# Optimization experiments

Measured on AMD Instinct MI355X. Metric: run time of the kernel, lower is better.

The kernel has to match this reference:

```python
import jax, jax.numpy as jnp
import numpy as np

LOSS_WEIGHT = 1.0


def _pairwise_l1(x, y):
    # x: [B, N, 3], y: [B, M, 3] -> d: [B, N, M] with d[b,i,j] = sum_k |x[b,i,k]-y[b,j,k]|
    # Loop over the fixed D=3 coordinate axis to avoid a [B,N,M,3] intermediate.
    d = jnp.abs(x[:, :, None, 0] - y[:, None, :, 0])
    for k in range(1, x.shape[-1]):
        d = d + jnp.abs(x[:, :, None, k] - y[:, None, :, k])
    return d


def setup_inputs() -> dict:
    key = jax.random.key(0)
    kx, ky = jax.random.split(key)
    mesh_x = jax.random.normal(kx, (4, 4096, 3), dtype=jnp.float32)
    mesh_y = jax.random.normal(ky, (4, 4096, 3), dtype=jnp.float32)
    return {"mesh_x": mesh_x, "mesh_y": mesh_y}


def reference(mesh_x, mesh_y):
    # pytorch3d chamfer_distance(norm=1), point_reduction='mean', batch_reduction='mean'
    d = _pairwise_l1(mesh_x, mesh_y)          # [B, N, M]
    cham_x = jnp.min(d, axis=2)               # [B, N] nearest y for each x
    cham_y = jnp.min(d, axis=1)               # [B, M] nearest x for each y
    # mean over points then mean over batch == global mean (uniform N, M)
    loss = jnp.mean(cham_x) + jnp.mean(cham_y)
    return LOSS_WEIGHT * loss
```

## Files before the change

kernel.cpp:

```cpp
#include <hip/hip_runtime.h>

#define BATCH 4
#define NPTS  4096
#define TPB   64
#define PPT   4
#define PB    (TPB * PPT)
#define QC    128
#define ZMAX  32

__device__ __forceinline__ void min3(float& m, float a, float b) {
    asm("v_min3_f32 %0, %0, %1, %2" : "+v"(m) : "v"(a), "v"(b));
}

__global__ __launch_bounds__(TPB) void chamfer_all(const float* __restrict__ X,
                                                   const float* __restrict__ Y,
                                                   float* __restrict__ pmin,
                                                   float* __restrict__ out,
                                                   int zsteps) {
    if (blockIdx.x == 0 && blockIdx.y == 0 && blockIdx.z == 0 && threadIdx.x == 0)
        out[0] = 0.0f;

    const int dir = blockIdx.y >> 2;
    const int b   = blockIdx.y & 3;
    const int z   = blockIdx.z;
    const float* __restrict__ P = dir ? Y : X;
    const float* __restrict__ Q = dir ? X : Y;

    float px[PPT], py[PPT], pz[PPT], m[PPT];
    const int i0 = blockIdx.x * PB + threadIdx.x;
    #pragma unroll
    for (int u = 0; u < PPT; ++u) {
        const float* Pp = P + ((size_t)b * NPTS + i0 + u * TPB) * 3;
        px[u] = Pp[0];
        py[u] = Pp[1];
        pz[u] = Pp[2];
        m[u]  = __builtin_inff();
    }

    __shared__ float4 sq[QC];
    const int q0 = z * zsteps * QC;

    for (int s = 0; s < zsteps; ++s) {
        __syncthreads();
        const float* __restrict__ Qb = Q + ((size_t)b * NPTS + q0 + s * QC) * 3;
        for (int k = threadIdx.x; k < QC; k += TPB)
            sq[k] = make_float4(Qb[3 * k], Qb[3 * k + 1], Qb[3 * k + 2], 0.0f);
        __syncthreads();

        #pragma unroll 4
        for (int j = 0; j < QC; j += 2) {
            const float4 qa = sq[j];
            const float4 qb = sq[j + 1];
            #pragma unroll
            for (int u = 0; u < PPT; ++u) {
                float d0 = fabsf(px[u] - qa.x) + fabsf(py[u] - qa.y) + fabsf(pz[u] - qa.z);
                float d1 = fabsf(px[u] - qb.x) + fabsf(py[u] - qb.y) + fabsf(pz[u] - qb.z);
                min3(m[u], d0, d1);
            }
        }
    }

    float* dst = pmin + ((size_t)dir * gridDim.z + z) * (BATCH * NPTS) + b * NPTS + i0;
    #pragma unroll
    for (int u = 0; u < PPT; ++u) dst[u * TPB] = m[u];
}

__global__ __launch_bounds__(256) void reduce_loss(const float* __restrict__ pmin,
                                                   float* __restrict__ out, int Z) {
    const int half = BATCH * NPTS;
    const int s    = blockIdx.x * 256 + threadIdx.x;
    const int dir  = s >> 14;
    const int idx  = s & (half - 1);

    const float* __restrict__ base = pmin + (size_t)dir * Z * half + idx;
    float v = base[0];
    for (int z = 1; z < Z; ++z) v = fminf(v, base[(size_t)z * half]);

    for (int off = 32; off > 0; off >>= 1) v += __shfl_down(v, off, 64);

    __shared__ float partial[4];
    if ((threadIdx.x & 63) == 0) partial[threadIdx.x >> 6] = v;
    __syncthreads();
    if (threadIdx.x == 0) {
        float t = (partial[0] + partial[1] + partial[2] + partial[3]) *
                  (1.0f / (float)half);
        atomicAdd(out, t);
    }
}

extern "C" void kernel_launch(void* const* d_in, const int* in_sizes, int n_in,
                              void* d_out, int out_size, void* d_ws, size_t ws_size,
                              hipStream_t stream) {
    const float* X = (const float*)d_in[0];
    const float* Y = (const float*)d_in[1];
    float* out = (float*)d_out;
    float* pmin = (float*)d_ws;

    int Z = ZMAX;
    while (Z > 1 && (size_t)2 * Z * BATCH * NPTS * sizeof(float) > ws_size) Z >>= 1;
    const int zsteps = ZMAX / Z;

    dim3 grid(NPTS / PB, 2 * BATCH, Z);
    chamfer_all<<<grid, TPB, 0, stream>>>(X, Y, pmin, out, zsteps);

    reduce_loss<<<(2 * BATCH * NPTS) / 256, 256, 0, stream>>>(pmin, out, Z);
}
```

Before: 78.32 us.

## Fuse chamfer min and loss reduction into one kernel with last-block finalize

Replaces the two-kernel design (per-slice partial mins written to workspace, then a reduce kernel) with one kernel. Each 512-thread block covers 64 points against all query slices, split across 32 groups of 16 threads. The groups combine through shared-memory atomicMin, and a last-block-done counter performs the final sum. Query points are read directly from global memory as packed float4 instead of being staged in LDS. The distance uses v_add_f32 with abs modifiers. This removes the pmin workspace traffic and the second launch, at the cost of a memset launch, uncoalesced/redundant global Q reads, and an atomic counter.

```diff
diff --git a/kernel.cpp b/kernel.cpp
--- a/kernel.cpp
+++ b/kernel.cpp
@@ -2,89 +2,112 @@
 
 #define BATCH 4
 #define NPTS  4096
-#define TPB   64
+#define TPB   512
+#define PC    64
+#define NPG   16
 #define PPT   4
-#define PB    (TPB * PPT)
-#define QC    128
-#define ZMAX  32
+#define NZZ   32
+#define QSL   (NPTS / NZZ)
+#define NBLK  (2 * BATCH * (NPTS / PC))
 
 __device__ __forceinline__ void min3(float& m, float a, float b) {
     asm("v_min3_f32 %0, %0, %1, %2" : "+v"(m) : "v"(a), "v"(b));
 }
+__device__ __forceinline__ float add_abs2(float a, float b) {
+    float d;
+    asm("v_add_f32 %0, |%1|, |%2|" : "=v"(d) : "v"(a), "v"(b));
+    return d;
+}
+__device__ __forceinline__ float add_abs1(float acc, float c) {
+    float d;
+    asm("v_add_f32 %0, %1, |%2|" : "=v"(d) : "v"(acc), "v"(c));
+    return d;
+}
 
-__global__ __launch_bounds__(TPB) void chamfer_all(const float* __restrict__ X,
-                                                   const float* __restrict__ Y,
-                                                   float* __restrict__ pmin,
-                                                   float* __restrict__ out,
-                                                   int zsteps) {
-    if (blockIdx.x == 0 && blockIdx.y == 0 && blockIdx.z == 0 && threadIdx.x == 0)
-        out[0] = 0.0f;
-
-    const int dir = blockIdx.y >> 2;
-    const int b   = blockIdx.y & 3;
-    const int z   = blockIdx.z;
-    const float* __restrict__ P = dir ? Y : X;
-    const float* __restrict__ Q = dir ? X : Y;
-
-    float px[PPT], py[PPT], pz[PPT], m[PPT];
-    const int i0 = blockIdx.x * PB + threadIdx.x;
+__device__ __forceinline__ void dist4x4(const float4 g0, const float4 g1,
+                                        const float4 g2, const float px[PPT],
+                                        const float py[PPT], const float pz[PPT],
+                                        float m[PPT]) {
     #pragma unroll
     for (int u = 0; u < PPT; ++u) {
-        const float* Pp = P + ((size_t)b * NPTS + i0 + u * TPB) * 3;
-        px[u] = Pp[0];
-        py[u] = Pp[1];
-        pz[u] = Pp[2];
-        m[u]  = __builtin_inff();
+        float dA = add_abs1(add_abs2(px[u] - g0.x, py[u] - g0.y), pz[u] - g0.z);
+        float dB = add_abs1(add_abs2(px[u] - g0.w, py[u] - g1.x), pz[u] - g1.y);
+        float dC = add_abs1(add_abs2(px[u] - g1.z, py[u] - g1.w), pz[u] - g2.x);
+        float dD = add_abs1(add_abs2(px[u] - g2.y, py[u] - g2.z), pz[u] - g2.w);
+        min3(m[u], dA, dB);
+        min3(m[u], dC, dD);
+    }
+}
+
+__global__ __launch_bounds__(TPB) void chamfer_fused(const float* __restrict__ X,
+                                                     const float* __restrict__ Y,
+                                                     unsigned int* __restrict__ cnt,
+                                                     float* __restrict__ psum,
+                                                     float* __restrict__ out) {
+    const int t   = threadIdx.x;
+    const int pg  = t & (NPG - 1);
+    const int zz  = t >> 4;
+    const int bid = blockIdx.x;
+    const int x   = bid & 63;
+    const int db  = bid >> 6;
+    const int b   = db & 3;
+    const float* __restrict__ P = (db >> 2) ? Y : X;
+    const float* __restrict__ Q = (db >> 2) ? X : Y;
+
+    const float4* __restrict__ Ps =
+        (const float4*)(P + ((size_t)b * NPTS + x * PC + pg * PPT) * 3);
+    const float4 f0 = Ps[0], f1 = Ps[1], f2 = Ps[2];
+    float px[PPT], py[PPT], pz[PPT], m[PPT];
+    px[0]=f0.x; py[0]=f0.y; pz[0]=f0.z;  px[1]=f0.w; py[1]=f1.x; pz[1]=f1.y;
+    px[2]=f1.z; py[2]=f1.w; pz[2]=f2.x;  px[3]=f2.y; py[3]=f2.z; pz[3]=f2.w;
+    #pragma unroll
+    for (int u = 0; u < PPT; ++u) m[u] = __builtin_inff();
+
+    const float4* __restrict__ Qs =
+        (const float4*)(Q + ((size_t)b * NPTS + zz * QSL) * 3);
+    #pragma unroll 4
+    for (int j = 0; j < (QSL / 4) * 3; j += 3) {
+        const float4 g0 = Qs[j], g1 = Qs[j + 1], g2 = Qs[j + 2];
+        dist4x4(g0, g1, g2, px, py, pz, m);
     }
 
-    __shared__ float4 sq[QC];
-    const int q0 = z * zsteps * QC;
+    __shared__ unsigned int smin[PC];
+    __shared__ int lastf;
+    if (t < PC) smin[t] = 0x7F800000u;
+    __syncthreads();
+    #pragma unroll
+    for (int u = 0; u < PPT; ++u)
+        atomicMin(&smin[pg * PPT + u], __float_as_uint(m[u]));
+    __syncthreads();
 
-    for (int s = 0; s < zsteps; ++s) {
-        __syncthreads();
-        const float* __restrict__ Qb = Q + ((size_t)b * NPTS + q0 + s * QC) * 3;
-        for (int k = threadIdx.x; k < QC; k += TPB)
-            sq[k] = make_float4(Qb[3 * k], Qb[3 * k + 1], Qb[3 * k + 2], 0.0f);
-        __syncthreads();
-
-        #pragma unroll 4
-        for (int j = 0; j < QC; j += 2) {
-            const float4 qa = sq[j];
-            const float4 qb = sq[j + 1];
-            #pragma unroll
-            for (int u = 0; u < PPT; ++u) {
-                float d0 = fabsf(px[u] - qa.x) + fabsf(py[u] - qa.y) + fabsf(pz[u] - qa.z);
-                float d1 = fabsf(px[u] - qb.x) + fabsf(py[u] - qb.y) + fabsf(pz[u] - qb.z);
-                min3(m[u], d0, d1);
-            }
+    if (t < 64) {
+        float v = __uint_as_float(smin[t]);
+        #pragma unroll
+        for (int off = 32; off > 0; off >>= 1) v += __shfl_down(v, off, 64);
+        if (t == 0) {
+            __hip_atomic_store(&psum[bid], v, __ATOMIC_RELEASE,
+                               __HIP_MEMORY_SCOPE_AGENT);
+            unsigned int old = __hip_atomic_fetch_add(
+                cnt, 1u, __ATOMIC_ACQ_REL, __HIP_MEMORY_SCOPE_AGENT);
+            lastf = (old == NBLK - 1);
         }
     }
+    __syncthreads();
 
-    float* dst = pmin + ((size_t)dir * gridDim.z + z) * (BATCH * NPTS) + b * NPTS + i0;
-    #pragma unroll
-    for (int u = 0; u < PPT; ++u) dst[u * TPB] = m[u];
-}
-
-__global__ __launch_bounds__(256) void reduce_loss(const float* __restrict__ pmin,
-                                                   float* __restrict__ out, int Z) {
-    const int half = BATCH * NPTS;
-    const int s    = blockIdx.x * 256 + threadIdx.x;
-    const int dir  = s >> 14;
-    const int idx  = s & (half - 1);
-
-    const float* __restrict__ base = pmin + (size_t)dir * Z * half + idx;
-    float v = base[0];
-    for (int z = 1; z < Z; ++z) v = fminf(v, base[(size_t)z * half]);
-
-    for (int off = 32; off > 0; off >>= 1) v += __shfl_down(v, off, 64);
-
-    __shared__ float partial[4];
-    if ((threadIdx.x & 63) == 0) partial[threadIdx.x >> 6] = v;
-    __syncthreads();
-    if (threadIdx.x == 0) {
-        float t = (partial[0] + partial[1] + partial[2] + partial[3]) *
-                  (1.0f / (float)half);
-        atomicAdd(out, t);
+    if (lastf) {
+        float s = __hip_atomic_load(&psum[t], __ATOMIC_ACQUIRE,
+                                    __HIP_MEMORY_SCOPE_AGENT);
+        #pragma unroll
+        for (int off = 32; off > 0; off >>= 1) s += __shfl_down(s, off, 64);
+        __shared__ float wsum[TPB / 64];
+        if ((t & 63) == 0) wsum[t >> 6] = s;
+        __syncthreads();
+        if (t == 0) {
+            float tot = 0.f;
+            #pragma unroll
+            for (int w = 0; w < TPB / 64; ++w) tot += wsum[w];
+            out[0] = tot * (1.0f / (float)(BATCH * NPTS));
+        }
     }
 }
 
@@ -94,14 +117,10 @@
     const float* X = (const float*)d_in[0];
     const float* Y = (const float*)d_in[1];
     float* out = (float*)d_out;
-    float* pmin = (float*)d_ws;
 
-    int Z = ZMAX;
-    while (Z > 1 && (size_t)2 * Z * BATCH * NPTS * sizeof(float) > ws_size) Z >>= 1;
-    const int zsteps = ZMAX / Z;
+    unsigned int* cnt = (unsigned int*)d_ws;
+    float* psum = (float*)d_ws + 16;
 
-    dim3 grid(NPTS / PB, 2 * BATCH, Z);
-    chamfer_all<<<grid, TPB, 0, stream>>>(X, Y, pmin, out, zsteps);
-
-    reduce_loss<<<(2 * BATCH * NPTS) / 256, 256, 0, stream>>>(pmin, out, Z);
+    hipMemsetAsync(cnt, 0, sizeof(unsigned int), stream);
+    chamfer_fused<<<NBLK, TPB, 0, stream>>>(X, Y, cnt, psum, out);
 }
```

After: 83.73 us. 1.07x slower.
